# Kernel tuning notes

Measured on AMD Instinct MI355X. Metric: run time of the kernel, lower is better.

Reference implementation:

```python
import jax, jax.numpy as jnp
import numpy as np

B, TP, TF, C, H, W = 8, 3, 4, 256, 64, 64
BN_EPS = 1e-3  # YOLOX BaseConv BatchNorm2d eps


def setup_inputs() -> dict:
    key = jax.random.key(0)
    ks = jax.random.split(key, 12)
    s = 1.0 / np.sqrt(C)
    return {
        "feature": jax.random.normal(ks[0], (B, TP + 1, C, H, W), jnp.float32),
        "past_time_constant": jax.random.normal(ks[1], (B, TP), jnp.float32),
        "future_time_constant": jax.random.normal(ks[2], (B, TF), jnp.float32),
        # fc_time_constant: Linear(1, C)
        "w_tc": jax.random.normal(ks[3], (C, 1), jnp.float32),
        "b_tc": jax.random.normal(ks[4], (C,), jnp.float32) * 0.1,
        # fc_in: Linear(2C, C)
        "w_in": jax.random.normal(ks[5], (C, 2 * C), jnp.float32) * (1.0 / np.sqrt(2 * C)),
        "b_in": jnp.zeros((C,), jnp.float32),
        # conv_p: 1x1 conv (no bias) + BN + SiLU
        "conv_w": jax.random.normal(ks[6], (C, C), jnp.float32) * s,
        "bn_gamma": jnp.ones((C,), jnp.float32),
        "bn_beta": jnp.zeros((C,), jnp.float32),
        "bn_mean": jax.random.normal(ks[7], (C,), jnp.float32) * 0.1,
        "bn_var": jnp.ones((C,), jnp.float32) + jax.random.uniform(ks[8], (C,)) * 0.1,
        # fc_query / fc_key: Linear(C, C)
        "w_q": jax.random.normal(ks[9], (C, C), jnp.float32) * s,
        "b_q": jnp.zeros((C,), jnp.float32),
        "w_k": jax.random.normal(ks[10], (C, C), jnp.float32) * s,
        "b_k": jnp.zeros((C,), jnp.float32),
        # p_attn: [1,1,C,1,1]
        "p_attn": jnp.ones((1, 1, C, 1, 1), jnp.float32),
    }


def reference(feature, past_time_constant, future_time_constant,
              w_tc, b_tc, w_in, b_in, conv_w, bn_gamma, bn_beta, bn_mean, bn_var,
              w_q, b_q, w_k, b_k, p_attn):
    b, t1, c, h, w = feature.shape
    tp = past_time_constant.shape[1]
    tf = future_time_constant.shape[1]
    silu = jax.nn.silu

    # conv_p = 1x1 conv (bias=False) + BatchNorm(eval) + SiLU, over all TP+1 frames
    x = jnp.einsum('oc,btchw->btohw', conv_w, feature)
    scale = bn_gamma / jnp.sqrt(bn_var + BN_EPS)          # [C]
    x = x * scale[:, None, None] + (bn_beta - bn_mean * scale)[:, None, None]
    feature_p = silu(x)                                    # [B,TP+1,C,H,W]

    # time-constant embeddings: tanh(Linear(1->C))
    ptc = jnp.tanh(past_time_constant[..., None] * w_tc[:, 0] + b_tc)    # [B,TP,C]
    ftc = jnp.tanh(future_time_constant[..., None] * w_tc[:, 0] + b_tc)  # [B,TF,C]

    # past branch: global max+avg pool over HxW, concat, fc_in+SiLU, add ptc
    fp_past = feature_p[:, :-1]                            # [B,TP,C,H,W]
    pool_p = jnp.concatenate([fp_past.max(axis=(-2, -1)), fp_past.mean(axis=(-2, -1))], axis=-1)  # [B,TP,2C]
    attn_in_p = silu(jnp.einsum('oc,btc->bto', w_in, pool_p) + b_in) + ptc  # [B,TP,C]

    # future branch: feature_f = last raw frame broadcast over TF (pool identical per TF)
    last = feature[:, -1]                                  # [B,C,H,W]
    pool_f = jnp.concatenate([last.max(axis=(-2, -1)), last.mean(axis=(-2, -1))], axis=-1)  # [B,2C]
    attn_in_f = silu(pool_f @ w_in.T + b_in)[:, None, :] + ftc  # [B,TF,C]

    q = attn_in_f @ w_q.T + b_q                            # [B,TF,C]
    k = attn_in_p @ w_k.T + b_k                            # [B,TP,C]
    v = (feature_p[:, -1:] - fp_past).reshape(b, tp, c * h * w)  # [B,TP,CHW]

    # NOTE: torch code scales by sqrt(attn_query.size(1)) == sqrt(TF), not sqrt(C)
    attn_w = jnp.einsum('bfc,bpc->bfp', q, k) / jnp.sqrt(jnp.asarray(tf, q.dtype))  # [B,TF,TP]
    attn = jnp.einsum('bfp,bpd->bfd', attn_w, v).reshape(b, tf, c, h, w)

    # residual: feature_f + attn * p_attn / attn_key.size(1) (== TP)
    out = last[:, None] + attn * p_attn / tp               # [B,TF,C,H,W]
    return out
```

## Files before the change

### kernel.cpp

```cpp
#include <hip/hip_runtime.h>

#define B_   8
#define T1_  4
#define TP_  3
#define TF_  4
#define C_   256
#define HW_  4096

#define OFF_FP     0ull
#define OFF_PMAXK  67108864ull
#define OFF_PSUM   67133440ull
#define OFF_RMAX   67158016ull
#define OFF_RSUM   67166208ull
#define OFF_Q      67174400ull
#define OFF_K      67207168ull
#define OFF_AW     67231744ull

typedef __attribute__((ext_vector_type(8))) short bf16x8;
typedef __attribute__((ext_vector_type(4))) float f32x4;

__device__ __forceinline__ unsigned short f2bf(float f) {
    unsigned int u = __float_as_uint(f);
    u += 0x7fffu + ((u >> 16) & 1u);
    return (unsigned short)(u >> 16);
}
__device__ __forceinline__ unsigned int fkey(float x) {
    unsigned int b = __float_as_uint(x);
    return (b & 0x80000000u) ? ~b : (b | 0x80000000u);
}
__device__ __forceinline__ float funkey(unsigned int k) {
    unsigned int b = (k & 0x80000000u) ? (k ^ 0x80000000u) : ~k;
    return __uint_as_float(b);
}
__device__ __forceinline__ float silu_f(float x) { return x / (1.0f + __expf(-x)); }

__device__ __forceinline__ void dec8(uint4 u, float* f) {
    f[0] = __uint_as_float(u.x << 16); f[1] = __uint_as_float(u.x & 0xffff0000u);
    f[2] = __uint_as_float(u.y << 16); f[3] = __uint_as_float(u.y & 0xffff0000u);
    f[4] = __uint_as_float(u.z << 16); f[5] = __uint_as_float(u.z & 0xffff0000u);
    f[6] = __uint_as_float(u.w << 16); f[7] = __uint_as_float(u.w & 0xffff0000u);
}

__global__ __launch_bounds__(256) void k0_rawpool(const float* __restrict__ feature,
                                                  float* __restrict__ rmax,
                                                  float* __restrict__ rsum) {
    const int blk = blockIdx.x;
    const int b = blk >> 8, c = blk & 255;
    const float* base = feature + ((size_t)(b * 4 + 3) * C_ + c) * HW_;
    const int tid = threadIdx.x;
    float mx = -3.4e38f, sm = 0.0f;
    #pragma unroll
    for (int k = 0; k < 4; ++k) {
        float4 v = *(const float4*)(base + (k * 256 + tid) * 4);
        mx = fmaxf(mx, fmaxf(fmaxf(v.x, v.y), fmaxf(v.z, v.w)));
        sm += (v.x + v.y) + (v.z + v.w);
    }
    #pragma unroll
    for (int m = 1; m < 64; m <<= 1) {
        mx = fmaxf(mx, __shfl_xor(mx, m));
        sm += __shfl_xor(sm, m);
    }
    __shared__ float wmx[4], wsm[4];
    const int wave = tid >> 6;
    if ((tid & 63) == 0) { wmx[wave] = mx; wsm[wave] = sm; }
    __syncthreads();
    if (tid == 0) {
        rmax[b * C_ + c] = fmaxf(fmaxf(wmx[0], wmx[1]), fmaxf(wmx[2], wmx[3]));
        rsum[b * C_ + c] = (wsm[0] + wsm[1]) + (wsm[2] + wsm[3]);
    }
}

__global__ __launch_bounds__(256) void k1_conv(
    const float* __restrict__ feature, const float* __restrict__ Wc,
    const float* __restrict__ gamma, const float* __restrict__ beta,
    const float* __restrict__ mean, const float* __restrict__ var,
    unsigned short* __restrict__ fp_out,
    unsigned int* __restrict__ pmaxk, float* __restrict__ psum) {
    __shared__ __align__(16) char smem[34816];
    unsigned short* lds_a = (unsigned short*)smem;
    unsigned short* lds_b = (unsigned short*)(smem + 20480);
    float* s_scale = (float*)(smem + 25600);
    float* s_shift = (float*)(smem + 26624);

    const int tid   = threadIdx.x;
    const int bt    = blockIdx.x >> 6;
    const int hwblk = blockIdx.x & 63;
    const int b = bt >> 2, t = bt & 3;
    const int hw0 = hwblk * 64;
    const int lane = tid & 63;
    const int wave = tid >> 6;
    const int q = lane >> 4;
    const int col = lane & 15;
    const int kg  = tid >> 6;
    const int hwl = tid & 63;

    {
        float sc = gamma[tid] * rsqrtf(var[tid] + 1e-3f);
        s_scale[tid] = sc;
        s_shift[tid] = beta[tid] - mean[tid] * sc;
    }

    const float* Fb = feature + (size_t)bt * C_ * HW_;
    f32x4 acc[4][4] = {};

    for (int k0 = 0; k0 < C_; k0 += 32) {
        __syncthreads();
        #pragma unroll
        for (int it = 0; it < 8; ++it) {
            int p = it * 256 + tid;
            int ol = p >> 3, cq = p & 7;
            float4 v = *(const float4*)(Wc + ol * 256 + k0 + cq * 4);
            ushort4 u;
            u.x = f2bf(v.x); u.y = f2bf(v.y); u.z = f2bf(v.z); u.w = f2bf(v.w);
            *(ushort4*)&lds_a[ol * 40 + cq * 4] = u;
        }
        {
            float fv[8];
            #pragma unroll
            for (int j = 0; j < 8; ++j)
                fv[j] = Fb[(size_t)(k0 + kg * 8 + j) * HW_ + hw0 + hwl];
            uint4 pk;
            pk.x = ((unsigned)f2bf(fv[1]) << 16) | f2bf(fv[0]);
            pk.y = ((unsigned)f2bf(fv[3]) << 16) | f2bf(fv[2]);
            pk.z = ((unsigned)f2bf(fv[5]) << 16) | f2bf(fv[4]);
            pk.w = ((unsigned)f2bf(fv[7]) << 16) | f2bf(fv[6]);
            *(uint4*)&lds_b[hwl * 40 + kg * 8] = pk;
        }
        __syncthreads();
        bf16x8 afr[4], bfr[4];
        #pragma unroll
        for (int mi = 0; mi < 4; ++mi)
            afr[mi] = *(const bf16x8*)&lds_a[(wave * 64 + mi * 16 + col) * 40 + q * 8];
        #pragma unroll
        for (int ni = 0; ni < 4; ++ni)
            bfr[ni] = *(const bf16x8*)&lds_b[(ni * 16 + col) * 40 + q * 8];
        #pragma unroll
        for (int mi = 0; mi < 4; ++mi)
            #pragma unroll
            for (int ni = 0; ni < 4; ++ni)
                acc[mi][ni] = __builtin_amdgcn_mfma_f32_16x16x32_bf16(afr[mi], bfr[ni], acc[mi][ni], 0, 0, 0);
    }

    unsigned short* fpo = fp_out + (size_t)bt * C_ * HW_;
    float pmx_r[16], psm_r[16];
    #pragma unroll
    for (int mi = 0; mi < 4; ++mi) {
        #pragma unroll
        for (int r = 0; r < 4; ++r) {
            const int o = wave * 64 + mi * 16 + q * 4 + r;
            const float sc = s_scale[o], sh = s_shift[o];
            float mx = -3.4e38f, sm = 0.0f;
            #pragma unroll
            for (int ni = 0; ni < 4; ++ni) {
                float x = acc[mi][ni][r] * sc + sh;
                float s = silu_f(x);
                fpo[(size_t)o * HW_ + hw0 + ni * 16 + col] = f2bf(s);
                mx = fmaxf(mx, s);
                sm += s;
            }
            pmx_r[mi * 4 + r] = mx;
            psm_r[mi * 4 + r] = sm;
        }
    }
    if (t < 3) {
        __syncthreads();
        float* pmx = (float*)smem;
        float* psm = (float*)(smem + 17408);
        #pragma unroll
        for (int mi = 0; mi < 4; ++mi)
            #pragma unroll
            for (int r = 0; r < 4; ++r) {
                const int o = wave * 64 + mi * 16 + q * 4 + r;
                pmx[o * 17 + col] = pmx_r[mi * 4 + r];
                psm[o * 17 + col] = psm_r[mi * 4 + r];
            }
        __syncthreads();
        const int o = tid;
        float m = pmx[o * 17], s2 = psm[o * 17];
        #pragma unroll
        for (int cc = 1; cc < 16; ++cc) {
            m = fmaxf(m, pmx[o * 17 + cc]);
            s2 += psm[o * 17 + cc];
        }
        atomicMax(&pmaxk[(b * 3 + t) * C_ + o], fkey(m));
        atomicAdd(&psum[(b * 3 + t) * C_ + o], s2);
    }
}

__global__ __launch_bounds__(256) void k2_vec(
    const float* __restrict__ past_tc, const float* __restrict__ fut_tc,
    const float* __restrict__ w_tc, const float* __restrict__ b_tc,
    const float* __restrict__ w_in, const float* __restrict__ b_in,
    const float* __restrict__ w_q, const float* __restrict__ b_q,
    const float* __restrict__ w_k, const float* __restrict__ b_k,
    const unsigned int* __restrict__ pmaxk, const float* __restrict__ psum,
    const float* __restrict__ rmax, const float* __restrict__ rsum,
    float* __restrict__ qout, float* __restrict__ kout) {
    __shared__ float pool[512];
    __shared__ float avec[256];
    const int b = blockIdx.x / 7;
    const int idx = blockIdx.x % 7;
    const int o = threadIdx.x;
    const bool pside = (idx < 3);
    if (pside) {
        pool[o]       = funkey(pmaxk[(b * 3 + idx) * C_ + o]);
        pool[256 + o] = psum[(b * 3 + idx) * C_ + o] * (1.0f / 4096.0f);
    } else {
        pool[o]       = rmax[b * C_ + o];
        pool[256 + o] = rsum[b * C_ + o] * (1.0f / 4096.0f);
    }
    __syncthreads();
    float s = b_in[o];
    const float* wr = w_in + (size_t)o * 512;
    #pragma unroll 8
    for (int c = 0; c < 512; ++c) s += wr[c] * pool[c];
    float v = silu_f(s);
    float tcin = pside ? past_tc[b * 3 + idx] : fut_tc[b * 4 + (idx - 3)];
    float tc = tanhf(tcin * w_tc[o] + b_tc[o]);
    avec[o] = v + tc;
    __syncthreads();
    if (pside) {
        float s2 = b_k[o];
        const float* wk = w_k + (size_t)o * 256;
        #pragma unroll 8
        for (int c = 0; c < 256; ++c) s2 += wk[c] * avec[c];
        kout[(b * 3 + idx) * C_ + o] = s2;
    } else {
        float s2 = b_q[o];
        const float* wq = w_q + (size_t)o * 256;
        #pragma unroll 8
        for (int c = 0; c < 256; ++c) s2 += wq[c] * avec[c];
        qout[(b * 4 + (idx - 3)) * C_ + o] = s2;
    }
}

__global__ __launch_bounds__(64) void k2_attnw(const float* __restrict__ qv,
                                               const float* __restrict__ kv,
                                               float* __restrict__ aw) {
    const int i = blockIdx.x;
    const int b = i / 12, rr = i % 12, f = rr / 3, p = rr % 3;
    const int lane = threadIdx.x;
    const float* qp = qv + (b * 4 + f) * C_;
    const float* kp = kv + (b * 3 + p) * C_;
    float s = 0.0f;
    #pragma unroll
    for (int j = 0; j < 4; ++j) s += qp[lane + 64 * j] * kp[lane + 64 * j];
    #pragma unroll
    for (int m = 1; m < 64; m <<= 1) s += __shfl_xor(s, m);
    if (lane == 0) aw[b * 12 + rr] = s * 0.5f;
}

__global__ __launch_bounds__(256) void k3_out(
    const float* __restrict__ feature, const unsigned short* __restrict__ fp,
    const float* __restrict__ aw, const float* __restrict__ p_attn,
    float* __restrict__ out) {
    const int idx = blockIdx.x;
    const int b = idx >> 9;
    const int c = (idx >> 1) & 255;
    const int half = idx & 1;
    const int hw = half * 2048 + threadIdx.x * 8;

    float a[12];
    #pragma unroll
    for (int i = 0; i < 12; ++i) a[i] = aw[b * 12 + i];
    const float pa = p_attn[c] * (1.0f / 3.0f);

    const size_t ts = (size_t)C_ * HW_;
    const size_t base = ((size_t)(b * 4) * C_ + c) * HW_ + hw;

    uint4 u0 = *(const uint4*)(fp + base);
    uint4 u1 = *(const uint4*)(fp + base + ts);
    uint4 u2 = *(const uint4*)(fp + base + 2 * ts);
    uint4 u3 = *(const uint4*)(fp + base + 3 * ts);
    float4 l0 = *(const float4*)(feature + base + 3 * ts);
    float4 l1 = *(const float4*)(feature + base + 3 * ts + 4);

    float f0[8], f1[8], f2[8], f3[8];
    dec8(u0, f0); dec8(u1, f1); dec8(u2, f2); dec8(u3, f3);
    float lastv[8] = {l0.x, l0.y, l0.z, l0.w, l1.x, l1.y, l1.z, l1.w};

    float ov[4][8];
    #pragma unroll
    for (int e = 0; e < 8; ++e) {
        float d0 = f3[e] - f0[e];
        float d1 = f3[e] - f1[e];
        float d2 = f3[e] - f2[e];
        #pragma unroll
        for (int f = 0; f < 4; ++f) {
            float at = a[f * 3 + 0] * d0 + a[f * 3 + 1] * d1 + a[f * 3 + 2] * d2;
            ov[f][e] = lastv[e] + at * pa;
        }
    }
    #pragma unroll
    for (int f = 0; f < 4; ++f) {
        size_t ob = ((size_t)(b * 4 + f) * C_ + c) * HW_ + hw;
        *(float4*)(out + ob)     = make_float4(ov[f][0], ov[f][1], ov[f][2], ov[f][3]);
        *(float4*)(out + ob + 4) = make_float4(ov[f][4], ov[f][5], ov[f][6], ov[f][7]);
    }
}

extern "C" void kernel_launch(void* const* d_in, const int* in_sizes, int n_in,
                              void* d_out, int out_size, void* d_ws, size_t ws_size,
                              hipStream_t stream) {
    const float* feature = (const float*)d_in[0];
    const float* past_tc = (const float*)d_in[1];
    const float* fut_tc  = (const float*)d_in[2];
    const float* w_tc    = (const float*)d_in[3];
    const float* b_tc    = (const float*)d_in[4];
    const float* w_in    = (const float*)d_in[5];
    const float* b_in    = (const float*)d_in[6];
    const float* conv_w  = (const float*)d_in[7];
    const float* gamma   = (const float*)d_in[8];
    const float* beta    = (const float*)d_in[9];
    const float* mean    = (const float*)d_in[10];
    const float* var     = (const float*)d_in[11];
    const float* w_q     = (const float*)d_in[12];
    const float* b_q     = (const float*)d_in[13];
    const float* w_k     = (const float*)d_in[14];
    const float* b_k     = (const float*)d_in[15];
    const float* p_attn  = (const float*)d_in[16];

    char* ws = (char*)d_ws;
    unsigned short* fp  = (unsigned short*)(ws + OFF_FP);
    unsigned int* pmaxk = (unsigned int*)(ws + OFF_PMAXK);
    float* psum = (float*)(ws + OFF_PSUM);
    float* rmax = (float*)(ws + OFF_RMAX);
    float* rsum = (float*)(ws + OFF_RSUM);
    float* qout = (float*)(ws + OFF_Q);
    float* kout = (float*)(ws + OFF_K);
    float* aw   = (float*)(ws + OFF_AW);

    hipMemsetAsync(ws + OFF_PMAXK, 0, 49152, stream);

    k0_rawpool<<<B_ * C_, 256, 0, stream>>>(feature, rmax, rsum);
    k1_conv<<<B_ * T1_ * 64, 256, 0, stream>>>(feature, conv_w, gamma, beta, mean, var,
                                               fp, pmaxk, psum);
    k2_vec<<<B_ * 7, 256, 0, stream>>>(past_tc, fut_tc, w_tc, b_tc, w_in, b_in,
                                       w_q, b_q, w_k, b_k, pmaxk, psum, rmax, rsum,
                                       qout, kout);
    k2_attnw<<<B_ * TF_ * TP_, 64, 0, stream>>>(qout, kout, aw);
    k3_out<<<B_ * C_ * 2, 256, 0, stream>>>(feature, fp, aw, p_attn, (float*)d_out);
}
```

Baseline: 363.3 us.

## Prepack conv weights into MFMA fragments and prefetch next K-slice in conv kernel

Adds a small pre-kernel that converts the 1x1 conv weights to bf16 once, laid out in MFMA fragment order. The conv kernel then loads A fragments straight from global memory instead of staging and converting them through LDS in every block. It also prefetches the next K-slice of feature values and weights into registers while the MFMAs run, and uses the packed bf16 convert instruction. The pooled max/sum reduction moves from an LDS pass to wave shuffles with per-16-lane atomics. When the workspace is too small, the fragment buffer is placed in the tail of the output buffer, which adds register pressure and a dependency on output memory that is later overwritten.

```diff
diff --git a/kernel.cpp b/kernel.cpp
--- a/kernel.cpp
+++ b/kernel.cpp
@@ -15,6 +15,8 @@
 #define OFF_Q      67174400ull
 #define OFF_K      67207168ull
 #define OFF_AW     67231744ull
+#define OFF_WFRAG  67232128ull
+#define WS_NEED    67363200ull
 
 typedef __attribute__((ext_vector_type(8))) short bf16x8;
 typedef __attribute__((ext_vector_type(4))) float f32x4;
@@ -23,6 +25,11 @@
     unsigned int u = __float_as_uint(f);
     u += 0x7fffu + ((u >> 16) & 1u);
     return (unsigned short)(u >> 16);
+}
+__device__ __forceinline__ unsigned int cvtpk(float lo, float hi) {
+    unsigned int r;
+    asm("v_cvt_pk_bf16_f32 %0, %1, %2" : "=v"(r) : "v"(lo), "v"(hi));
+    return r;
 }
 __device__ __forceinline__ unsigned int fkey(float x) {
     unsigned int b = __float_as_uint(x);
@@ -39,6 +46,21 @@
     f[2] = __uint_as_float(u.y << 16); f[3] = __uint_as_float(u.y & 0xffff0000u);
     f[4] = __uint_as_float(u.z << 16); f[5] = __uint_as_float(u.z & 0xffff0000u);
     f[6] = __uint_as_float(u.w << 16); f[7] = __uint_as_float(u.w & 0xffff0000u);
+}
+
+__global__ __launch_bounds__(256) void k_wpre(const float* __restrict__ Wc,
+                                              unsigned short* __restrict__ wfrag) {
+    const int idx = blockIdx.x * 256 + threadIdx.x;
+    const int j   = idx & 7;
+    const int fi  = idx >> 3;
+    const int col = fi & 15;
+    const int q   = (fi >> 4) & 3;
+    const int sob = fi >> 6;
+    const int ob  = sob & 15;
+    const int s   = sob >> 4;
+    const int o   = ob * 16 + col;
+    const int c   = s * 32 + q * 8 + j;
+    wfrag[idx] = f2bf(Wc[o * 256 + c]);
 }
 
 __global__ __launch_bounds__(256) void k0_rawpool(const float* __restrict__ feature,
@@ -71,16 +93,14 @@
 }
 
 __global__ __launch_bounds__(256) void k1_conv(
-    const float* __restrict__ feature, const float* __restrict__ Wc,
+    const float* __restrict__ feature, const unsigned short* __restrict__ wfrag,
     const float* __restrict__ gamma, const float* __restrict__ beta,
     const float* __restrict__ mean, const float* __restrict__ var,
     unsigned short* __restrict__ fp_out,
     unsigned int* __restrict__ pmaxk, float* __restrict__ psum) {
-    __shared__ __align__(16) char smem[34816];
-    unsigned short* lds_a = (unsigned short*)smem;
-    unsigned short* lds_b = (unsigned short*)(smem + 20480);
-    float* s_scale = (float*)(smem + 25600);
-    float* s_shift = (float*)(smem + 26624);
+    __shared__ __align__(16) unsigned short lds_b[64 * 40];
+    __shared__ float s_scale[256];
+    __shared__ float s_shift[256];
 
     const int tid   = threadIdx.x;
     const int bt    = blockIdx.x >> 6;
@@ -91,7 +111,6 @@
     const int wave = tid >> 6;
     const int q = lane >> 4;
     const int col = lane & 15;
-    const int kg  = tid >> 6;
     const int hwl = tid & 63;
 
     {
@@ -103,46 +122,56 @@
     const float* Fb = feature + (size_t)bt * C_ * HW_;
     f32x4 acc[4][4] = {};
 
-    for (int k0 = 0; k0 < C_; k0 += 32) {
+    float fv[8];
+    #pragma unroll
+    for (int j = 0; j < 8; ++j)
+        fv[j] = Fb[(size_t)(wave * 8 + j) * HW_ + hw0 + hwl];
+    bf16x8 afr[4];
+    #pragma unroll
+    for (int mi = 0; mi < 4; ++mi)
+        afr[mi] = *(const bf16x8*)(wfrag + ((size_t)(wave * 4 + mi) * 64 + lane) * 8);
+
+    #pragma unroll
+    for (int s = 0; s < 8; ++s) {
         __syncthreads();
-        #pragma unroll
-        for (int it = 0; it < 8; ++it) {
-            int p = it * 256 + tid;
-            int ol = p >> 3, cq = p & 7;
-            float4 v = *(const float4*)(Wc + ol * 256 + k0 + cq * 4);
-            ushort4 u;
-            u.x = f2bf(v.x); u.y = f2bf(v.y); u.z = f2bf(v.z); u.w = f2bf(v.w);
-            *(ushort4*)&lds_a[ol * 40 + cq * 4] = u;
-        }
-        {
-            float fv[8];
-            #pragma unroll
-            for (int j = 0; j < 8; ++j)
-                fv[j] = Fb[(size_t)(k0 + kg * 8 + j) * HW_ + hw0 + hwl];
-            uint4 pk;
-            pk.x = ((unsigned)f2bf(fv[1]) << 16) | f2bf(fv[0]);
-            pk.y = ((unsigned)f2bf(fv[3]) << 16) | f2bf(fv[2]);
-            pk.z = ((unsigned)f2bf(fv[5]) << 16) | f2bf(fv[4]);
-            pk.w = ((unsigned)f2bf(fv[7]) << 16) | f2bf(fv[6]);
-            *(uint4*)&lds_b[hwl * 40 + kg * 8] = pk;
-        }
+        uint4 pk;
+        pk.x = cvtpk(fv[0], fv[1]);
+        pk.y = cvtpk(fv[2], fv[3]);
+        pk.z = cvtpk(fv[4], fv[5]);
+        pk.w = cvtpk(fv[6], fv[7]);
+        *(uint4*)&lds_b[hwl * 40 + wave * 8] = pk;
         __syncthreads();
-        bf16x8 afr[4], bfr[4];
-        #pragma unroll
-        for (int mi = 0; mi < 4; ++mi)
-            afr[mi] = *(const bf16x8*)&lds_a[(wave * 64 + mi * 16 + col) * 40 + q * 8];
+
+        bf16x8 bfr[4];
         #pragma unroll
         for (int ni = 0; ni < 4; ++ni)
             bfr[ni] = *(const bf16x8*)&lds_b[(ni * 16 + col) * 40 + q * 8];
+
+        bf16x8 afn[4];
+        if (s < 7) {
+            #pragma unroll
+            for (int j = 0; j < 8; ++j)
+                fv[j] = Fb[(size_t)((s + 1) * 32 + wave * 8 + j) * HW_ + hw0 + hwl];
+            #pragma unroll
+            for (int mi = 0; mi < 4; ++mi)
+                afn[mi] = *(const bf16x8*)(wfrag +
+                           ((size_t)((s + 1) * 16 + wave * 4 + mi) * 64 + lane) * 8);
+        }
+
         #pragma unroll
         for (int mi = 0; mi < 4; ++mi)
             #pragma unroll
             for (int ni = 0; ni < 4; ++ni)
-                acc[mi][ni] = __builtin_amdgcn_mfma_f32_16x16x32_bf16(afr[mi], bfr[ni], acc[mi][ni], 0, 0, 0);
+                acc[mi][ni] = __builtin_amdgcn_mfma_f32_16x16x32_bf16(
+                    afr[mi], bfr[ni], acc[mi][ni], 0, 0, 0);
+
+        if (s < 7) {
+            #pragma unroll
+            for (int mi = 0; mi < 4; ++mi) afr[mi] = afn[mi];
+        }
     }
 
     unsigned short* fpo = fp_out + (size_t)bt * C_ * HW_;
-    float pmx_r[16], psm_r[16];
     #pragma unroll
     for (int mi = 0; mi < 4; ++mi) {
         #pragma unroll
@@ -153,37 +182,23 @@
             #pragma unroll
             for (int ni = 0; ni < 4; ++ni) {
                 float x = acc[mi][ni][r] * sc + sh;
-                float s = silu_f(x);
-                fpo[(size_t)o * HW_ + hw0 + ni * 16 + col] = f2bf(s);
-                mx = fmaxf(mx, s);
-                sm += s;
+                float sl = silu_f(x);
+                fpo[(size_t)o * HW_ + hw0 + ni * 16 + col] = f2bf(sl);
+                mx = fmaxf(mx, sl);
+                sm += sl;
             }
-            pmx_r[mi * 4 + r] = mx;
-            psm_r[mi * 4 + r] = sm;
+            if (t < 3) {
+                #pragma unroll
+                for (int m = 1; m < 16; m <<= 1) {
+                    mx = fmaxf(mx, __shfl_xor(mx, m));
+                    sm += __shfl_xor(sm, m);
+                }
+                if (col == 0) {
+                    atomicMax(&pmaxk[(b * 3 + t) * C_ + o], fkey(mx));
+                    atomicAdd(&psum[(b * 3 + t) * C_ + o], sm);
+                }
+            }
         }
-    }
-    if (t < 3) {
-        __syncthreads();
-        float* pmx = (float*)smem;
-        float* psm = (float*)(smem + 17408);
-        #pragma unroll
-        for (int mi = 0; mi < 4; ++mi)
-            #pragma unroll
-            for (int r = 0; r < 4; ++r) {
-                const int o = wave * 64 + mi * 16 + q * 4 + r;
-                pmx[o * 17 + col] = pmx_r[mi * 4 + r];
-                psm[o * 17 + col] = psm_r[mi * 4 + r];
-            }
-        __syncthreads();
-        const int o = tid;
-        float m = pmx[o * 17], s2 = psm[o * 17];
-        #pragma unroll
-        for (int cc = 1; cc < 16; ++cc) {
-            m = fmaxf(m, pmx[o * 17 + cc]);
-            s2 += psm[o * 17 + cc];
-        }
-        atomicMax(&pmaxk[(b * 3 + t) * C_ + o], fkey(m));
-        atomicAdd(&psum[(b * 3 + t) * C_ + o], s2);
     }
 }
 
@@ -329,11 +344,15 @@
     float* qout = (float*)(ws + OFF_Q);
     float* kout = (float*)(ws + OFF_K);
     float* aw   = (float*)(ws + OFF_AW);
+    unsigned short* wfrag = (ws_size >= WS_NEED)
+        ? (unsigned short*)(ws + OFF_WFRAG)
+        : (unsigned short*)((char*)d_out + (size_t)out_size - 131072);
 
     hipMemsetAsync(ws + OFF_PMAXK, 0, 49152, stream);
 
+    k_wpre<<<256, 256, 0, stream>>>(conv_w, wfrag);
     k0_rawpool<<<B_ * C_, 256, 0, stream>>>(feature, rmax, rsum);
-    k1_conv<<<B_ * T1_ * 64, 256, 0, stream>>>(feature, conv_w, gamma, beta, mean, var,
+    k1_conv<<<B_ * T1_ * 64, 256, 0, stream>>>(feature, wfrag, gamma, beta, mean, var,
                                                fp, pmaxk, psum);
     k2_vec<<<B_ * 7, 256, 0, stream>>>(past_tc, fut_tc, w_tc, b_tc, w_in, b_in,
                                        w_q, b_q, w_k, b_k, pmaxk, psum, rmax, rsum,
```

Result: faster. 350.7 us (-3.5%).
